# Kernel tuning notes

Measured on AMD Instinct MI355X. Metric: run time of the kernel, lower is better.

## Reference

```python
import jax, jax.numpy as jnp
import numpy as np

B, T, H, D = 1, 2048, 32, 128
Q_GROUP = 4
HKV = H // Q_GROUP
INNER = H * D
KV_INNER = HKV * D
ROPE_BASE = 10000.0
NEG = -1e30


def _rope_tables(seq_len, head_dim, dtype):
    inv_freq = 1.0 / (ROPE_BASE ** (jnp.arange(0, head_dim, 2, dtype=jnp.float32) / head_dim))
    t = jnp.arange(seq_len, dtype=jnp.float32)
    freqs = jnp.einsum('t,f->tf', t, inv_freq)          # [T, D/2]
    emb = jnp.concatenate([freqs, freqs], axis=-1)      # [T, D]
    cos = jnp.cos(emb)[None, :, None, :].astype(dtype)  # [1, T, 1, D]
    sin = jnp.sin(emb)[None, :, None, :].astype(dtype)
    return cos, sin


def _rotate(x, cos, sin):
    # x: [B, T, H, D]; split-half rotation: cat(-x2, x1)
    half = x.shape[-1] // 2
    x1, x2 = x[..., :half], x[..., half:]
    x_rot = jnp.concatenate([-x2, x1], axis=-1)
    return x * cos + x_rot * sin


def setup_inputs() -> dict:
    key = jax.random.key(0)
    ks = jax.random.split(key, 5)
    return {
        'stm': jax.random.normal(ks[0], (B, T, H, D), dtype=jnp.float32),
        'w_q': jax.random.normal(ks[1], (INNER, INNER), dtype=jnp.float32) * 0.02,
        'w_k': jax.random.normal(ks[2], (KV_INNER, INNER), dtype=jnp.float32) * 0.02,
        'w_v': jax.random.normal(ks[3], (KV_INNER, INNER), dtype=jnp.float32) * 0.02,
        'w_o': jax.random.normal(ks[4], (INNER, INNER), dtype=jnp.float32) * 0.02,
    }


def reference(stm, w_q, w_k, w_v, w_o):
    b, t, h, d = stm.shape
    x = stm.reshape(b * t, h * d)
    q = x @ w_q.T                                   # [B*T, H*D]
    k = x @ w_k.T                                   # [B*T, Hkv*D]
    v = x @ w_v.T
    # GQA repeat_interleave over query-group axis (broadcast then reshape)
    k = jnp.broadcast_to(k.reshape(b * t, HKV, 1, d), (b * t, HKV, Q_GROUP, d)).reshape(b, t, h, d)
    v = jnp.broadcast_to(v.reshape(b * t, HKV, 1, d), (b * t, HKV, Q_GROUP, d)).reshape(b, t, h, d)
    q = q.reshape(b, t, h, d)
    cos, sin = _rope_tables(t, d, stm.dtype)        # prefill: seq_start = 0
    q = _rotate(q, cos, sin)
    k = _rotate(k, cos, sin)                        # rotated k is what gets written to the KV cache
    scale = 1.0 / np.sqrt(d)
    scores = jnp.einsum('bqhd,bkhd->bhqk', q, k).astype(jnp.float32) * scale
    causal = jnp.tril(jnp.ones((t, t), dtype=jnp.float32))          # mask_w
    bias = (1.0 - causal) * NEG                                     # mask_b
    scores = scores * causal[None, None] + bias[None, None]
    attn = jax.nn.softmax(scores, axis=-1).astype(stm.dtype)
    o = jnp.einsum('bhqk,bkhd->bqhd', attn, v)
    o = o.reshape(b * t, h * d) @ w_o.T
    return o.reshape(b, t, h, d)
```

## Files before the change

### kernel.cpp

```cpp
#include <hip/hip_runtime.h>
#include <hip/hip_bf16.h>
#include <stdint.h>
#include <stddef.h>

using bf16  = __hip_bfloat16;
using v4s   = __attribute__((ext_vector_type(4))) short;
using v8s   = __attribute__((ext_vector_type(8))) short;
using f32x4 = __attribute__((ext_vector_type(4))) float;

#define MFMA_16x16x32(a, b, c) __builtin_amdgcn_mfma_f32_16x16x32_bf16((a), (b), (c), 0, 0, 0)

__device__ __forceinline__ void async_lds16(const bf16* g, bf16* l) {
  __builtin_amdgcn_global_load_lds(
      (const __attribute__((address_space(1))) void*)g,
      (__attribute__((address_space(3))) void*)l, 16, 0, 0);
}

__device__ __forceinline__ short bf16_bits(float f) {
  bf16 h = __float2bfloat16(f);
  short s;
  __builtin_memcpy(&s, &h, sizeof(s));
  return s;
}

__global__ void cvt_f32_bf16(const float* __restrict__ in, bf16* __restrict__ out,
                             int n4) {
  const int i = blockIdx.x * blockDim.x + threadIdx.x;
  if (i >= n4) return;
  const float4 f = ((const float4*)in)[i];
  v4s o;
  o[0] = bf16_bits(f.x);
  o[1] = bf16_bits(f.y);
  o[2] = bf16_bits(f.z);
  o[3] = bf16_bits(f.w);
  *(v4s*)(out + (size_t)i * 4) = o;
}

template <bool F32OUT>
__global__ __launch_bounds__(512, 2) void gemm_bt9(const bf16* __restrict__ A,
                                                   const bf16* __restrict__ B,
                                                   void* __restrict__ C,
                                                   int M, int N, int K) {
  __shared__ bf16 lds[2][64][512];
  const int tid  = threadIdx.x;
  const int w    = tid >> 6;
  const int lane = tid & 63;
  const int quad = lane >> 4;
  const int m16  = lane & 15;
  const int wr = w >> 2, wc = w & 3;
  const int tm = blockIdx.y, tn = blockIdx.x;
  const int NKT = K >> 6;

  const bf16* Ast0 = A + (size_t)(tm * 256 + w * 16 + m16) * K + quad * 8;
  const bf16* Ast1 = Ast0 + (size_t)128 * K;
  const bf16* Bst0 = B + (size_t)(tn * 256 + w * 16 + m16) * K + quad * 8;
  const bf16* Bst1 = Bst0 + (size_t)128 * K;

  auto stage = [&](const bf16* g, bf16* l) {
    async_lds16(g, l);
    async_lds16(g + 32, l + 512);
  };

  f32x4 acc[8][4] = {};
  v8s af[4][2];
  v8s bf01[2][2];
  v8s bf23[2][2];

  {
    bf16* L0 = &lds[0][0][0];
    bf16* L1 = &lds[1][0][0];
    stage(Bst0, L0 + (32 + w * 2) * 512);
    stage(Bst1, L0 + (48 + w * 2) * 512);
    stage(Ast0, L0 + (w * 2) * 512);
    stage(Ast1, L0 + (16 + w * 2) * 512);
    stage(Bst0 + 64, L1 + (32 + w * 2) * 512);
    stage(Bst1 + 64, L1 + (48 + w * 2) * 512);
    stage(Ast0 + 64, L1 + (w * 2) * 512);
  }
  asm volatile("s_waitcnt vmcnt(6)" ::: "memory");
  __builtin_amdgcn_s_barrier();
  {
    bf16* L0 = &lds[0][0][0];
#pragma unroll
    for (int mi = 0; mi < 4; ++mi)
#pragma unroll
      for (int kg = 0; kg < 2; ++kg)
        af[mi][kg] = *(const v8s*)(L0 + ((wr * 8 + mi) * 2 + kg) * 512 + lane * 8);
#pragma unroll
    for (int ni = 0; ni < 2; ++ni)
#pragma unroll
      for (int kg = 0; kg < 2; ++kg) {
        bf01[ni][kg] = *(const v8s*)(L0 + (32 + (wc * 4 + ni) * 2 + kg) * 512 + lane * 8);
        bf23[ni][kg] = *(const v8s*)(L0 + (32 + (wc * 4 + 2 + ni) * 2 + kg) * 512 + lane * 8);
      }
  }
  asm volatile("" ::: "memory");

  for (int k = 0; k < NKT; ++k) {
    bf16* Lc = &lds[k & 1][0][0];
    bf16* Ln = &lds[(k & 1) ^ 1][0][0];
    __builtin_amdgcn_s_barrier();
    if (k + 1 < NKT) stage(Ast1 + (size_t)(k + 1) * 64, Ln + (16 + w * 2) * 512);
    asm volatile("s_waitcnt lgkmcnt(0)" ::: "memory");
    __builtin_amdgcn_sched_barrier(0);
    __builtin_amdgcn_s_setprio(1);
#pragma unroll
    for (int mi = 0; mi < 4; ++mi)
#pragma unroll
      for (int ni = 0; ni < 2; ++ni) {
        acc[mi][ni] = MFMA_16x16x32(af[mi][0], bf01[ni][0], acc[mi][ni]);
        acc[mi][ni] = MFMA_16x16x32(af[mi][1], bf01[ni][1], acc[mi][ni]);
      }
    __builtin_amdgcn_s_setprio(0);
    asm volatile("" ::: "memory");
    __builtin_amdgcn_s_barrier();
    if (k + 2 < NKT) stage(Bst0 + (size_t)(k + 2) * 64, Lc + (32 + w * 2) * 512);
    __builtin_amdgcn_s_setprio(1);
#pragma unroll
    for (int mi = 0; mi < 4; ++mi)
#pragma unroll
      for (int ni = 0; ni < 2; ++ni) {
        acc[mi][2 + ni] = MFMA_16x16x32(af[mi][0], bf23[ni][0], acc[mi][2 + ni]);
        acc[mi][2 + ni] = MFMA_16x16x32(af[mi][1], bf23[ni][1], acc[mi][2 + ni]);
      }
    __builtin_amdgcn_s_setprio(0);
    asm volatile("" ::: "memory");
#pragma unroll
    for (int mi = 0; mi < 4; ++mi)
#pragma unroll
      for (int kg = 0; kg < 2; ++kg)
        af[mi][kg] = *(const v8s*)(Lc + ((wr * 8 + 4 + mi) * 2 + kg) * 512 + lane * 8);
    asm volatile("" ::: "memory");
    if (k + 2 < NKT) {
      asm volatile("s_waitcnt vmcnt(6)" ::: "memory");
    } else if (k + 1 < NKT) {
      asm volatile("s_waitcnt vmcnt(4)" ::: "memory");
    }
    __builtin_amdgcn_s_barrier();
    if (k + 2 < NKT) stage(Bst1 + (size_t)(k + 2) * 64, Lc + (48 + w * 2) * 512);
    asm volatile("s_waitcnt lgkmcnt(0)" ::: "memory");
    __builtin_amdgcn_sched_barrier(0);
    __builtin_amdgcn_s_setprio(1);
#pragma unroll
    for (int mi = 0; mi < 4; ++mi)
#pragma unroll
      for (int ni = 0; ni < 2; ++ni) {
        acc[4 + mi][2 + ni] = MFMA_16x16x32(af[mi][0], bf23[ni][0], acc[4 + mi][2 + ni]);
        acc[4 + mi][2 + ni] = MFMA_16x16x32(af[mi][1], bf23[ni][1], acc[4 + mi][2 + ni]);
      }
    __builtin_amdgcn_s_setprio(0);
    asm volatile("" ::: "memory");
    if (k + 1 < NKT) {
#pragma unroll
      for (int ni = 0; ni < 2; ++ni)
#pragma unroll
        for (int kg = 0; kg < 2; ++kg)
          bf23[ni][kg] = *(const v8s*)(Ln + (32 + (wc * 4 + 2 + ni) * 2 + kg) * 512 + lane * 8);
    }
    asm volatile("" ::: "memory");
    if (k + 2 < NKT) {
      asm volatile("s_waitcnt vmcnt(4)" ::: "memory");
    } else if (k + 1 < NKT) {
      asm volatile("s_waitcnt vmcnt(0)" ::: "memory");
    }
    __builtin_amdgcn_s_barrier();
    if (k + 2 < NKT) stage(Ast0 + (size_t)(k + 2) * 64, Lc + (w * 2) * 512);
    __builtin_amdgcn_s_setprio(1);
#pragma unroll
    for (int mi = 0; mi < 4; ++mi)
#pragma unroll
      for (int ni = 0; ni < 2; ++ni) {
        acc[4 + mi][ni] = MFMA_16x16x32(af[mi][0], bf01[ni][0], acc[4 + mi][ni]);
        acc[4 + mi][ni] = MFMA_16x16x32(af[mi][1], bf01[ni][1], acc[4 + mi][ni]);
      }
    __builtin_amdgcn_s_setprio(0);
    asm volatile("" ::: "memory");
    if (k + 1 < NKT) {
#pragma unroll
      for (int mi = 0; mi < 4; ++mi)
#pragma unroll
        for (int kg = 0; kg < 2; ++kg)
          af[mi][kg] = *(const v8s*)(Ln + ((wr * 8 + mi) * 2 + kg) * 512 + lane * 8);
#pragma unroll
      for (int ni = 0; ni < 2; ++ni)
#pragma unroll
        for (int kg = 0; kg < 2; ++kg)
          bf01[ni][kg] = *(const v8s*)(Ln + (32 + (wc * 4 + ni) * 2 + kg) * 512 + lane * 8);
    }
    asm volatile("" ::: "memory");
  }

#pragma unroll
  for (int mi = 0; mi < 8; ++mi)
#pragma unroll
    for (int ni = 0; ni < 4; ++ni) {
      const int row = tm * 256 + wr * 128 + mi * 16 + quad * 4;
      const int col = tn * 256 + wc * 64 + ni * 16 + m16;
#pragma unroll
      for (int r = 0; r < 4; ++r) {
        if (F32OUT)
          ((float*)C)[(size_t)(row + r) * N + col] = acc[mi][ni][r];
        else
          ((bf16*)C)[(size_t)(row + r) * N + col] = __float2bfloat16(acc[mi][ni][r]);
      }
    }
}

__global__ void rope_tab(float2* __restrict__ tab) {
  const int t = blockIdx.x;
  const int f = threadIdx.x;
  const float invf = powf(10000.0f, -(float)f * (1.0f / 64.0f));
  const float ang  = (float)t * invf;
  tab[t * 64 + f] = make_float2(cosf(ang), sinf(ang));
}

__global__ void rope_kernel(bf16* __restrict__ qkv, const float2* __restrict__ tab) {
  const int t  = blockIdx.x;
  const int hh = blockIdx.y;
  const int d  = threadIdx.x;
  const float2 cs = tab[t * 64 + (d & 63)];
  const float c = cs.x;
  const float s = cs.y;
  const bool isq = (hh < 32);
  bf16* ptr = qkv + (size_t)t * 6144 + (isq ? hh * 128 : 4096 + (hh - 32) * 128);
  const float x   = __bfloat162float(ptr[d]);
  const float xp  = __bfloat162float(ptr[d ^ 64]);
  __syncthreads();
  const float rot = (d < 64) ? -xp : xp;
  const float outv = (x * c + rot * s) * (isq ? 0.08838834764831845f : 1.0f);
  ptr[d] = __float2bfloat16(outv);
}

__global__ void vtrans_kernel(const bf16* __restrict__ qkv, bf16* __restrict__ vt) {
  __shared__ bf16 tile[32][34];
  const int t0 = blockIdx.x * 32, c0 = blockIdx.y * 32;
  const int tx = threadIdx.x, ty = threadIdx.y;
#pragma unroll
  for (int i = 0; i < 4; ++i)
    tile[ty + 8 * i][tx] = qkv[(size_t)(t0 + ty + 8 * i) * 6144 + 5120 + c0 + tx];
  __syncthreads();
#pragma unroll
  for (int i = 0; i < 4; ++i)
    vt[(size_t)(c0 + ty + 8 * i) * 2048 + t0 + tx] = tile[tx][ty + 8 * i];
}

__global__ __launch_bounds__(256) void attn_fused4(const bf16* __restrict__ QKV,
                                                   const bf16* __restrict__ Vt,
                                                   bf16* __restrict__ O) {
  const int bx = (int)blockIdx.x;
  const int h  = (int)blockIdx.y;
  const int qt = (h < 16) ? (15 - bx) : bx;
  const int hk = h >> 2;
  const int tid = threadIdx.x, w = tid >> 6, lane = tid & 63;
  const int quad = lane >> 4, m16 = lane & 15;
  __shared__ bf16 Ks[32 * 512];
  __shared__ bf16 Vs[32 * 512];
  __shared__ __attribute__((aligned(16))) short Ps[4][2048];
  short* Pw = Ps[w];

  v8s qf[2][4];
#pragma unroll
  for (int ni = 0; ni < 2; ++ni)
#pragma unroll
    for (int dk = 0; dk < 4; ++dk)
      qf[ni][dk] = *(const v8s*)(QKV + (size_t)(qt * 128 + w * 32 + ni * 16 + m16) * 6144 +
                                 h * 128 + dk * 32 + quad * 8);

  const bf16* kg = QKV + (size_t)m16 * 6144 + 4096 + hk * 128 + w * 32 + quad * 8;
  const bf16* vg = Vt + (size_t)(hk * 128 + m16) * 2048 + w * 32 + quad * 8;

  f32x4 acc[8][2] = {};
  float m_run[2] = {-1e30f, -1e30f}, l_run[2] = {0.f, 0.f};

#pragma unroll
  for (int mi = 0; mi < 8; ++mi)
    async_lds16(kg + (size_t)mi * 16 * 6144, &Ks[(mi * 4 + w) * 512]);
#pragma unroll
  for (int mi = 0; mi < 8; ++mi)
    async_lds16(vg + (size_t)mi * 16 * 2048, &Vs[(mi * 4 + w) * 512]);

  for (int kt = 0; kt <= qt; ++kt) {
    asm volatile("s_waitcnt vmcnt(8)" ::: "memory");
    __builtin_amdgcn_s_barrier();
    f32x4 s[8][2];
    __builtin_amdgcn_s_setprio(1);
#pragma unroll
    for (int mi = 0; mi < 8; ++mi) {
      s[mi][0] = f32x4{0.f, 0.f, 0.f, 0.f};
      s[mi][1] = f32x4{0.f, 0.f, 0.f, 0.f};
#pragma unroll
      for (int dk = 0; dk < 4; ++dk) {
        v8s af = *(const v8s*)&Ks[(mi * 4 + dk) * 512 + lane * 8];
        s[mi][0] = MFMA_16x16x32(af, qf[0][dk], s[mi][0]);
        s[mi][1] = MFMA_16x16x32(af, qf[1][dk], s[mi][1]);
      }
    }
    __builtin_amdgcn_s_setprio(0);
    asm volatile("s_waitcnt vmcnt(0)" ::: "memory");
    __builtin_amdgcn_s_barrier();
    if (kt < qt) {
      const bf16* kg2 = kg + (size_t)(kt + 1) * 128 * 6144;
#pragma unroll
      for (int mi = 0; mi < 8; ++mi)
        async_lds16(kg2 + (size_t)mi * 16 * 6144, &Ks[(mi * 4 + w) * 512]);
    }
    if (kt == qt) {
#pragma unroll
      for (int mi = 0; mi < 8; ++mi)
#pragma unroll
        for (int ni = 0; ni < 2; ++ni)
#pragma unroll
          for (int r = 0; r < 4; ++r)
            if (mi * 16 + quad * 4 + r > w * 32 + ni * 16 + m16) s[mi][ni][r] = -1e30f;
    }
#pragma unroll
    for (int ni = 0; ni < 2; ++ni) {
      float mx = -1e30f;
#pragma unroll
      for (int mi = 0; mi < 8; ++mi)
#pragma unroll
        for (int r = 0; r < 4; ++r) mx = fmaxf(mx, s[mi][ni][r]);
      mx = fmaxf(mx, __shfl_xor(mx, 16));
      mx = fmaxf(mx, __shfl_xor(mx, 32));
      const float mnew = fmaxf(m_run[ni], mx);
      const float alpha = __expf(m_run[ni] - mnew);
      m_run[ni] = mnew;
      float rs = 0.f;
#pragma unroll
      for (int mi = 0; mi < 8; ++mi)
#pragma unroll
        for (int r = 0; r < 4; ++r) {
          const float p = __expf(s[mi][ni][r] - mnew);
          s[mi][ni][r] = p;
          rs += p;
        }
      rs += __shfl_xor(rs, 16);
      rs += __shfl_xor(rs, 32);
      l_run[ni] = l_run[ni] * alpha + rs;
#pragma unroll
      for (int mi2 = 0; mi2 < 8; ++mi2)
#pragma unroll
        for (int r = 0; r < 4; ++r) acc[mi2][ni][r] *= alpha;
    }
#pragma unroll
    for (int mi = 0; mi < 4; ++mi)
#pragma unroll
      for (int ni = 0; ni < 2; ++ni) {
        v4s p4;
#pragma unroll
        for (int r = 0; r < 4; ++r) p4[r] = bf16_bits(s[mi][ni][r]);
        const int base = (ni * 2 + (mi >> 1)) * 512 +
                         ((mi & 1) * 2 + (quad >> 1)) * 128 + m16 * 8 + (quad & 1) * 4;
        *(v4s*)&Pw[base] = p4;
      }
    asm volatile("" ::: "memory");
    __builtin_amdgcn_s_setprio(1);
#pragma unroll
    for (int kpl = 0; kpl < 2; ++kpl) {
      v8s pf0 = *(const v8s*)&Pw[(0 * 2 + kpl) * 512 + lane * 8];
      v8s pf1 = *(const v8s*)&Pw[(1 * 2 + kpl) * 512 + lane * 8];
#pragma unroll
      for (int mi2 = 0; mi2 < 8; ++mi2) {
        v8s vf = *(const v8s*)&Vs[(mi2 * 4 + kpl) * 512 + lane * 8];
        acc[mi2][0] = MFMA_16x16x32(vf, pf0, acc[mi2][0]);
        acc[mi2][1] = MFMA_16x16x32(vf, pf1, acc[mi2][1]);
      }
    }
    __builtin_amdgcn_s_setprio(0);
    asm volatile("" ::: "memory");
#pragma unroll
    for (int mi = 4; mi < 8; ++mi)
#pragma unroll
      for (int ni = 0; ni < 2; ++ni) {
        const int mloc = mi - 4;
        v4s p4;
#pragma unroll
        for (int r = 0; r < 4; ++r) p4[r] = bf16_bits(s[mi][ni][r]);
        const int base = (ni * 2 + (mloc >> 1)) * 512 +
                         ((mloc & 1) * 2 + (quad >> 1)) * 128 + m16 * 8 + (quad & 1) * 4;
        *(v4s*)&Pw[base] = p4;
      }
    asm volatile("" ::: "memory");
    __builtin_amdgcn_s_setprio(1);
#pragma unroll
    for (int kpl = 0; kpl < 2; ++kpl) {
      v8s pf0 = *(const v8s*)&Pw[(0 * 2 + kpl) * 512 + lane * 8];
      v8s pf1 = *(const v8s*)&Pw[(1 * 2 + kpl) * 512 + lane * 8];
#pragma unroll
      for (int mi2 = 0; mi2 < 8; ++mi2) {
        v8s vf = *(const v8s*)&Vs[(mi2 * 4 + 2 + kpl) * 512 + lane * 8];
        acc[mi2][0] = MFMA_16x16x32(vf, pf0, acc[mi2][0]);
        acc[mi2][1] = MFMA_16x16x32(vf, pf1, acc[mi2][1]);
      }
    }
    __builtin_amdgcn_s_setprio(0);
    asm volatile("" ::: "memory");
    __builtin_amdgcn_s_barrier();
    if (kt < qt) {
      const bf16* vg2 = vg + (size_t)(kt + 1) * 128;
#pragma unroll
      for (int mi = 0; mi < 8; ++mi)
        async_lds16(vg2 + (size_t)mi * 16 * 2048, &Vs[(mi * 4 + w) * 512]);
    }
  }
#pragma unroll
  for (int ni = 0; ni < 2; ++ni) {
    const float rl = 1.0f / l_run[ni];
    const size_t qrow = qt * 128 + w * 32 + ni * 16 + m16;
#pragma unroll
    for (int mi2 = 0; mi2 < 8; ++mi2) {
      v4s o4;
#pragma unroll
      for (int r = 0; r < 4; ++r) o4[r] = bf16_bits(acc[mi2][ni][r] * rl);
      *(v4s*)(O + qrow * 4096 + h * 128 + mi2 * 16 + quad * 4) = o4;
    }
  }
}

extern "C" void kernel_launch(void* const* d_in, const int* in_sizes, int n_in,
                              void* d_out, int out_size, void* d_ws, size_t ws_size,
                              hipStream_t stream) {
  const float* stm = (const float*)d_in[0];
  const float* w_q = (const float*)d_in[1];
  const float* w_k = (const float*)d_in[2];
  const float* w_v = (const float*)d_in[3];
  const float* w_o = (const float*)d_in[4];
  float* out = (float*)d_out;

  const size_t M_STM = (size_t)2048 * 4096;
  const size_t M_WQ  = (size_t)4096 * 4096;
  const size_t M_WK  = (size_t)1024 * 4096;

  bf16* ws      = (bf16*)d_ws;
  bf16* wqkv_bf = ws;
  bf16* wo_bf   = ws;
  bf16* vT      = ws + M_WQ;
  float2* ropeT = (float2*)(ws + 18 * 1024 * 1024);
  bf16* stm_bf  = ws + 24 * 1024 * 1024;
  bf16* o_buf   = stm_bf;
  bf16* qkv_buf = ws + 32 * 1024 * 1024;

  cvt_f32_bf16<<<(int)(M_STM / 1024), 256, 0, stream>>>(stm, stm_bf, (int)(M_STM / 4));
  cvt_f32_bf16<<<(int)(M_WQ / 1024), 256, 0, stream>>>(w_q, wqkv_bf, (int)(M_WQ / 4));
  cvt_f32_bf16<<<(int)(M_WK / 1024), 256, 0, stream>>>(w_k, wqkv_bf + M_WQ, (int)(M_WK / 4));
  cvt_f32_bf16<<<(int)(M_WK / 1024), 256, 0, stream>>>(w_v, wqkv_bf + M_WQ + M_WK, (int)(M_WK / 4));

  gemm_bt9<false><<<dim3(24, 8), 512, 0, stream>>>(stm_bf, wqkv_bf, qkv_buf, 2048, 6144, 4096);

  cvt_f32_bf16<<<(int)(M_WQ / 1024), 256, 0, stream>>>(w_o, wo_bf, (int)(M_WQ / 4));
  rope_tab<<<2048, 64, 0, stream>>>(ropeT);

  rope_kernel<<<dim3(2048, 40), 128, 0, stream>>>(qkv_buf, ropeT);
  vtrans_kernel<<<dim3(64, 32), dim3(32, 8), 0, stream>>>(qkv_buf, vT);
  attn_fused4<<<dim3(16, 32), 256, 0, stream>>>(qkv_buf, vT, o_buf);

  gemm_bt9<true><<<dim3(16, 8), 512, 0, stream>>>(o_buf, wo_bf, out, 2048, 4096, 4096);
}
```

Measured before the change: 607.0 us.

## Restructure GEMM k-loop to load fragments from current LDS buffer with more barriers

The GEMM main loop no longer prefetches A/B register fragments from the next LDS buffer during compute. Each quarter-step now reads fragments from the current buffer, issues the next async global-to-LDS stage, then synchronises with extra barriers before its MFMA block. The vmcnt waits are simplified to a single wait before the last quarter. This may simplify hazards and scheduling, but it adds barriers and exposes LDS read latency that the old register prefetch hid.

```diff
diff --git a/kernel.cpp b/kernel.cpp
--- a/kernel.cpp
+++ b/kernel.cpp
@@ -37,10 +37,10 @@
 }
 
 template <bool F32OUT>
-__global__ __launch_bounds__(512, 2) void gemm_bt9(const bf16* __restrict__ A,
-                                                   const bf16* __restrict__ B,
-                                                   void* __restrict__ C,
-                                                   int M, int N, int K) {
+__global__ __launch_bounds__(512, 2) void gemm_bt11(const bf16* __restrict__ A,
+                                                    const bf16* __restrict__ B,
+                                                    void* __restrict__ C,
+                                                    int M, int N, int K) {
   __shared__ bf16 lds[2][64][512];
   const int tid  = threadIdx.x;
   const int w    = tid >> 6;
@@ -62,9 +62,6 @@
   };
 
   f32x4 acc[8][4] = {};
-  v8s af[4][2];
-  v8s bf01[2][2];
-  v8s bf23[2][2];
 
   {
     bf16* L0 = &lds[0][0][0];
@@ -79,30 +76,24 @@
   }
   asm volatile("s_waitcnt vmcnt(6)" ::: "memory");
   __builtin_amdgcn_s_barrier();
-  {
-    bf16* L0 = &lds[0][0][0];
-#pragma unroll
-    for (int mi = 0; mi < 4; ++mi)
-#pragma unroll
-      for (int kg = 0; kg < 2; ++kg)
-        af[mi][kg] = *(const v8s*)(L0 + ((wr * 8 + mi) * 2 + kg) * 512 + lane * 8);
-#pragma unroll
-    for (int ni = 0; ni < 2; ++ni)
-#pragma unroll
-      for (int kg = 0; kg < 2; ++kg) {
-        bf01[ni][kg] = *(const v8s*)(L0 + (32 + (wc * 4 + ni) * 2 + kg) * 512 + lane * 8);
-        bf23[ni][kg] = *(const v8s*)(L0 + (32 + (wc * 4 + 2 + ni) * 2 + kg) * 512 + lane * 8);
-      }
-  }
-  asm volatile("" ::: "memory");
 
   for (int k = 0; k < NKT; ++k) {
     bf16* Lc = &lds[k & 1][0][0];
     bf16* Ln = &lds[(k & 1) ^ 1][0][0];
-    __builtin_amdgcn_s_barrier();
+    v8s af[4][2], bf01[2][2], bf23[2][2];
+#pragma unroll
+    for (int mi = 0; mi < 4; ++mi)
+#pragma unroll
+      for (int kg = 0; kg < 2; ++kg)
+        af[mi][kg] = *(const v8s*)(Lc + ((wr * 8 + mi) * 2 + kg) * 512 + lane * 8);
+#pragma unroll
+    for (int ni = 0; ni < 2; ++ni)
+#pragma unroll
+      for (int kg = 0; kg < 2; ++kg)
+        bf01[ni][kg] = *(const v8s*)(Lc + (32 + (wc * 4 + ni) * 2 + kg) * 512 + lane * 8);
     if (k + 1 < NKT) stage(Ast1 + (size_t)(k + 1) * 64, Ln + (16 + w * 2) * 512);
+    __builtin_amdgcn_s_barrier();
     asm volatile("s_waitcnt lgkmcnt(0)" ::: "memory");
-    __builtin_amdgcn_sched_barrier(0);
     __builtin_amdgcn_s_setprio(1);
 #pragma unroll
     for (int mi = 0; mi < 4; ++mi)
@@ -112,9 +103,15 @@
         acc[mi][ni] = MFMA_16x16x32(af[mi][1], bf01[ni][1], acc[mi][ni]);
       }
     __builtin_amdgcn_s_setprio(0);
-    asm volatile("" ::: "memory");
-    __builtin_amdgcn_s_barrier();
+    __builtin_amdgcn_s_barrier();
+#pragma unroll
+    for (int ni = 0; ni < 2; ++ni)
+#pragma unroll
+      for (int kg = 0; kg < 2; ++kg)
+        bf23[ni][kg] = *(const v8s*)(Lc + (32 + (wc * 4 + 2 + ni) * 2 + kg) * 512 + lane * 8);
     if (k + 2 < NKT) stage(Bst0 + (size_t)(k + 2) * 64, Lc + (32 + w * 2) * 512);
+    __builtin_amdgcn_s_barrier();
+    asm volatile("s_waitcnt lgkmcnt(0)" ::: "memory");
     __builtin_amdgcn_s_setprio(1);
 #pragma unroll
     for (int mi = 0; mi < 4; ++mi)
@@ -124,22 +121,15 @@
         acc[mi][2 + ni] = MFMA_16x16x32(af[mi][1], bf23[ni][1], acc[mi][2 + ni]);
       }
     __builtin_amdgcn_s_setprio(0);
-    asm volatile("" ::: "memory");
+    __builtin_amdgcn_s_barrier();
 #pragma unroll
     for (int mi = 0; mi < 4; ++mi)
 #pragma unroll
       for (int kg = 0; kg < 2; ++kg)
         af[mi][kg] = *(const v8s*)(Lc + ((wr * 8 + 4 + mi) * 2 + kg) * 512 + lane * 8);
-    asm volatile("" ::: "memory");
-    if (k + 2 < NKT) {
-      asm volatile("s_waitcnt vmcnt(6)" ::: "memory");
-    } else if (k + 1 < NKT) {
-      asm volatile("s_waitcnt vmcnt(4)" ::: "memory");
-    }
-    __builtin_amdgcn_s_barrier();
     if (k + 2 < NKT) stage(Bst1 + (size_t)(k + 2) * 64, Lc + (48 + w * 2) * 512);
+    __builtin_amdgcn_s_barrier();
     asm volatile("s_waitcnt lgkmcnt(0)" ::: "memory");
-    __builtin_amdgcn_sched_barrier(0);
     __builtin_amdgcn_s_setprio(1);
 #pragma unroll
     for (int mi = 0; mi < 4; ++mi)
@@ -149,22 +139,14 @@
         acc[4 + mi][2 + ni] = MFMA_16x16x32(af[mi][1], bf23[ni][1], acc[4 + mi][2 + ni]);
       }
     __builtin_amdgcn_s_setprio(0);
-    asm volatile("" ::: "memory");
-    if (k + 1 < NKT) {
-#pragma unroll
-      for (int ni = 0; ni < 2; ++ni)
-#pragma unroll
-        for (int kg = 0; kg < 2; ++kg)
-          bf23[ni][kg] = *(const v8s*)(Ln + (32 + (wc * 4 + 2 + ni) * 2 + kg) * 512 + lane * 8);
-    }
-    asm volatile("" ::: "memory");
-    if (k + 2 < NKT) {
-      asm volatile("s_waitcnt vmcnt(4)" ::: "memory");
-    } else if (k + 1 < NKT) {
+    __builtin_amdgcn_s_barrier();
+    if (k + 2 < NKT) stage(Ast0 + (size_t)(k + 2) * 64, Lc + (w * 2) * 512);
+    if (k < NKT - 2) {
+      asm volatile("s_waitcnt vmcnt(6)" ::: "memory");
+    } else {
       asm volatile("s_waitcnt vmcnt(0)" ::: "memory");
     }
     __builtin_amdgcn_s_barrier();
-    if (k + 2 < NKT) stage(Ast0 + (size_t)(k + 2) * 64, Lc + (w * 2) * 512);
     __builtin_amdgcn_s_setprio(1);
 #pragma unroll
     for (int mi = 0; mi < 4; ++mi)
@@ -174,20 +156,7 @@
         acc[4 + mi][ni] = MFMA_16x16x32(af[mi][1], bf01[ni][1], acc[4 + mi][ni]);
       }
     __builtin_amdgcn_s_setprio(0);
-    asm volatile("" ::: "memory");
-    if (k + 1 < NKT) {
-#pragma unroll
-      for (int mi = 0; mi < 4; ++mi)
-#pragma unroll
-        for (int kg = 0; kg < 2; ++kg)
-          af[mi][kg] = *(const v8s*)(Ln + ((wr * 8 + mi) * 2 + kg) * 512 + lane * 8);
-#pragma unroll
-      for (int ni = 0; ni < 2; ++ni)
-#pragma unroll
-        for (int kg = 0; kg < 2; ++kg)
-          bf01[ni][kg] = *(const v8s*)(Ln + (32 + (wc * 4 + ni) * 2 + kg) * 512 + lane * 8);
-    }
-    asm volatile("" ::: "memory");
+    __builtin_amdgcn_s_barrier();
   }
 
 #pragma unroll
@@ -445,7 +414,7 @@
   cvt_f32_bf16<<<(int)(M_WK / 1024), 256, 0, stream>>>(w_k, wqkv_bf + M_WQ, (int)(M_WK / 4));
   cvt_f32_bf16<<<(int)(M_WK / 1024), 256, 0, stream>>>(w_v, wqkv_bf + M_WQ + M_WK, (int)(M_WK / 4));
 
-  gemm_bt9<false><<<dim3(24, 8), 512, 0, stream>>>(stm_bf, wqkv_bf, qkv_buf, 2048, 6144, 4096);
+  gemm_bt11<false><<<dim3(24, 8), 512, 0, stream>>>(stm_bf, wqkv_bf, qkv_buf, 2048, 6144, 4096);
 
   cvt_f32_bf16<<<(int)(M_WQ / 1024), 256, 0, stream>>>(w_o, wo_bf, (int)(M_WQ / 4));
   rope_tab<<<2048, 64, 0, stream>>>(ropeT);
@@ -454,5 +423,5 @@
   vtrans_kernel<<<dim3(64, 32), dim3(32, 8), 0, stream>>>(qkv_buf, vT);
   attn_fused4<<<dim3(16, 32), 256, 0, stream>>>(qkv_buf, vT, o_buf);
 
-  gemm_bt9<true><<<dim3(16, 8), 512, 0, stream>>>(o_buf, wo_bf, out, 2048, 4096, 4096);
-}
+  gemm_bt11<true><<<dim3(16, 8), 512, 0, stream>>>(o_buf, wo_bf, out, 2048, 4096, 4096);
+}
```

Measured after the change: 605.1 us. No clear change (-0.3%).
